# Kernel tuning notes

Measured on AMD Instinct MI355X. Metric: run time of the kernel, lower is better.

The kernel has to match this reference:

```python
import jax, jax.numpy as jnp
import numpy as np

EPS = 1e-6

def setup_inputs() -> dict:
    key = jax.random.key(0)
    k1, k2, k3 = jax.random.split(key, 3)
    B, C, H, W = 2048, 256, 7, 7
    base = jax.random.normal(k1, (B, C, H, W), dtype=jnp.float32)
    moment = jax.random.normal(k2, (B, C, H, W), dtype=jnp.float32)
    A_matrix = jax.random.randint(k3, (B, H * W, H * W), 0, 2, dtype=jnp.int32)
    return {"base": base, "moment": moment, "A_matrix": A_matrix}

def reference(base, moment, A_matrix):
    B, C, H, W = base.shape
    P = H * W  # 49
    b = base.reshape(B, C, P)      # (B, C, 49)
    m = moment.reshape(B, C, P)    # (B, C, 49)
    # pairwise dot over channel dim via batched matmul (avoids BxCx49x49 broadcast)
    dots = jnp.einsum('bcp,bcq->bpq', b, m)            # (B, 49, 49)
    nb = jnp.maximum(jnp.linalg.norm(b, axis=1), EPS)  # (B, 49)
    nm = jnp.maximum(jnp.linalg.norm(m, axis=1), EPS)  # (B, 49)
    cos_sim = dots / (nb[:, :, None] * nm[:, None, :])
    mask = A_matrix.astype(bool)
    # masked mean without dynamic-size gather
    num = jnp.sum(jnp.where(mask, cos_sim, 0.0))
    den = jnp.sum(mask).astype(cos_sim.dtype)
    return -(num / den)
```

## Files before the change

### kernel.cpp

```cpp
#include <hip/hip_runtime.h>
#include <hip/hip_bf16.h>
#include <stdint.h>


typedef __attribute__((ext_vector_type(8))) short short8;
typedef __attribute__((ext_vector_type(4))) float floatx4;

#define P 49
#define CP 12544
#define NMASK 2401
#define MS_STRIDE 72

__device__ __forceinline__ short8 cvt8(float4 a, float4 b) {
  union { __hip_bfloat162 h2; short s2[2]; } t;
  short8 r;
  t.h2 = __float22bfloat162_rn(make_float2(a.x, a.y)); r[0] = t.s2[0]; r[1] = t.s2[1];
  t.h2 = __float22bfloat162_rn(make_float2(a.z, a.w)); r[2] = t.s2[0]; r[3] = t.s2[1];
  t.h2 = __float22bfloat162_rn(make_float2(b.x, b.y)); r[4] = t.s2[0]; r[5] = t.s2[1];
  t.h2 = __float22bfloat162_rn(make_float2(b.z, b.w)); r[6] = t.s2[0]; r[7] = t.s2[1];
  return r;
}

__global__ __launch_bounds__(512, 6) void pixpro_main(
    const float* __restrict__ base, const float* __restrict__ moment,
    const int* __restrict__ A, float* __restrict__ ws_num, float* __restrict__ ws_cnt)
{
  __shared__ __align__(16) uint16_t maskS[P * MS_STRIDE];
  __shared__ __align__(16) float normred[8 * 4 * 64];
  __shared__ __align__(16) float inv_nm_s[64];
  __shared__ __align__(16) float SQred[8 * 4 * 16 * 2];
  __shared__ float cntred[8];

  const int b    = blockIdx.x;
  const int tid  = threadIdx.x;
  const int lane = tid & 63;
  const int wv   = tid >> 6;
  const int mrow = lane & 15;
  const int kgrp = (lane >> 4) & 3;

  const float* gb = base   + (size_t)b * CP;
  const float* gm = moment + (size_t)b * CP;
  const int*   gA = A      + (size_t)b * NMASK;

  short8 afrag[2][2];
  float s0[8], s1[8];
  #pragma unroll
  for (int j = 0; j < 8; ++j) { s0[j] = 0.f; s1[j] = 0.f; }

  #pragma unroll
  for (int cti = 0; cti < 2; ++cti) {
    const int c = (2 * wv + cti) * 16 + mrow;
    const float* row = gm + c * P;
    float4 a0 = *(const float4*)(row + kgrp * 8);
    float4 a1 = *(const float4*)(row + kgrp * 8 + 4);
    float4 b0, b1;
    if (kgrp < 2) {
      b0 = *(const float4*)(row + 32 + kgrp * 8);
      b1 = *(const float4*)(row + 32 + kgrp * 8 + 4);
    } else if (kgrp == 2) {
      b0 = make_float4(row[48], 0.f, 0.f, 0.f);
      b1 = make_float4(0.f, 0.f, 0.f, 0.f);
    } else {
      b0 = make_float4(0.f, 0.f, 0.f, 0.f);
      b1 = make_float4(0.f, 0.f, 0.f, 0.f);
    }
    s0[0] = fmaf(a0.x, a0.x, s0[0]); s0[1] = fmaf(a0.y, a0.y, s0[1]);
    s0[2] = fmaf(a0.z, a0.z, s0[2]); s0[3] = fmaf(a0.w, a0.w, s0[3]);
    s0[4] = fmaf(a1.x, a1.x, s0[4]); s0[5] = fmaf(a1.y, a1.y, s0[5]);
    s0[6] = fmaf(a1.z, a1.z, s0[6]); s0[7] = fmaf(a1.w, a1.w, s0[7]);
    s1[0] = fmaf(b0.x, b0.x, s1[0]); s1[1] = fmaf(b0.y, b0.y, s1[1]);
    s1[2] = fmaf(b0.z, b0.z, s1[2]); s1[3] = fmaf(b0.w, b0.w, s1[3]);
    s1[4] = fmaf(b1.x, b1.x, s1[4]); s1[5] = fmaf(b1.y, b1.y, s1[5]);
    s1[6] = fmaf(b1.z, b1.z, s1[6]); s1[7] = fmaf(b1.w, b1.w, s1[7]);
    afrag[cti][0] = cvt8(a0, a1);
    afrag[cti][1] = cvt8(b0, b1);
  }

  const bool btask = tid < P * 8;
  const int  bp    = tid >> 3;
  const int  bqg   = tid & 7;
  const int  bq0   = bqg * 8;
  int bmask[8];
  #pragma unroll
  for (int j = 0; j < 8; ++j) bmask[j] = 0;
  if (btask) {
    const int* Ar = gA + bp * P + bq0;
    if (bqg <= 5) {
      int4 u0 = *(const int4*)(Ar);
      int4 u1 = *(const int4*)(Ar + 4);
      bmask[0] = u0.x; bmask[1] = u0.y; bmask[2] = u0.z; bmask[3] = u0.w;
      bmask[4] = u1.x; bmask[5] = u1.y; bmask[6] = u1.z; bmask[7] = u1.w;
    } else if (bqg == 6) {
      bmask[0] = Ar[0];
    }
  }

  #pragma unroll
  for (int j = 0; j < 8; ++j) {
    s0[j] += __shfl_xor(s0[j], 1); s0[j] += __shfl_xor(s0[j], 2);
    s1[j] += __shfl_xor(s1[j], 1); s1[j] += __shfl_xor(s1[j], 2);
  }
  if ((lane & 3) == 0) {
    const int h = mrow >> 2;
    float* nb_ = &normred[(wv * 4 + h) * 64 + kgrp * 8];
    *(float4*)(nb_ + 0)  = make_float4(s0[0], s0[1], s0[2], s0[3]);
    *(float4*)(nb_ + 4)  = make_float4(s0[4], s0[5], s0[6], s0[7]);
    *(float4*)(nb_ + 32) = make_float4(s1[0], s1[1], s1[2], s1[3]);
    *(float4*)(nb_ + 36) = make_float4(s1[4], s1[5], s1[6], s1[7]);
  }
  __syncthreads();

  if (tid < 64) {
    float s = 0.f;
    #pragma unroll
    for (int wh = 0; wh < 32; ++wh) s += normred[wh * 64 + tid];
    inv_nm_s[tid] = 1.0f / fmaxf(sqrtf(s), 1e-6f);
  }
  __syncthreads();

  int cntpart = 0;
  if (btask) {
    float4 i0 = *(const float4*)&inv_nm_s[bq0];
    float4 i1 = *(const float4*)&inv_nm_s[bq0 + 4];
    float4 f0, f1;
    f0.x = bmask[0] ? i0.x : 0.f; f0.y = bmask[1] ? i0.y : 0.f;
    f0.z = bmask[2] ? i0.z : 0.f; f0.w = bmask[3] ? i0.w : 0.f;
    f1.x = bmask[4] ? i1.x : 0.f; f1.y = bmask[5] ? i1.y : 0.f;
    f1.z = bmask[6] ? i1.z : 0.f; f1.w = bmask[7] ? i1.w : 0.f;
    #pragma unroll
    for (int j = 0; j < 8; ++j) cntpart += bmask[j];
    *(short8*)&maskS[bp * MS_STRIDE + bq0] = cvt8(f0, f1);
  }
  __syncthreads();

  const int pbase[4] = {0, 16, 32, 33};
  floatx4 acc[2][4];
  #pragma unroll
  for (int i = 0; i < 2; ++i)
    #pragma unroll
    for (int j = 0; j < 4; ++j) acc[i][j] = (floatx4){0.f, 0.f, 0.f, 0.f};

  #pragma unroll
  for (int kt = 0; kt < 2; ++kt) {
    short8 bfr[4];
    #pragma unroll
    for (int pt = 0; pt < 4; ++pt)
      bfr[pt] = *(const short8*)&maskS[(pbase[pt] + mrow) * MS_STRIDE + kt * 32 + kgrp * 8];
    #pragma unroll
    for (int cti = 0; cti < 2; ++cti)
      #pragma unroll
      for (int pt = 0; pt < 4; ++pt)
        acc[cti][pt] = __builtin_amdgcn_mfma_f32_16x16x32_bf16(afrag[cti][kt], bfr[pt], acc[cti][pt], 0, 0, 0);
  }

  float S[4] = {0.f, 0.f, 0.f, 0.f}, Qn[4] = {0.f, 0.f, 0.f, 0.f};
  #pragma unroll
  for (int cti = 0; cti < 2; ++cti) {
    float bv[4][4];
    #pragma unroll
    for (int pt = 0; pt < 4; ++pt) {
      const int pd = pbase[pt] + mrow;
      const bool pv = (pt < 3) || (mrow == 15);
      #pragma unroll
      for (int r = 0; r < 4; ++r) {
        const int c = (2 * wv + cti) * 16 + kgrp * 4 + r;
        float v = gb[c * P + pd];
        bv[pt][r] = pv ? v : 0.f;
      }
    }
    #pragma unroll
    for (int pt = 0; pt < 4; ++pt)
      #pragma unroll
      for (int r = 0; r < 4; ++r) {
        S[pt]  = fmaf(bv[pt][r], acc[cti][pt][r], S[pt]);
        Qn[pt] = fmaf(bv[pt][r], bv[pt][r], Qn[pt]);
      }
  }

  #pragma unroll
  for (int pt = 0; pt < 4; ++pt) {
    S[pt]  += __shfl_xor(S[pt], 16);  S[pt]  += __shfl_xor(S[pt], 32);
    Qn[pt] += __shfl_xor(Qn[pt], 16); Qn[pt] += __shfl_xor(Qn[pt], 32);
  }
  float cntf = (float)cntpart;
  #pragma unroll
  for (int off = 32; off > 0; off >>= 1) cntf += __shfl_xor(cntf, off);

  if (lane < 16) {
    #pragma unroll
    for (int pt = 0; pt < 4; ++pt)
      *(float2*)&SQred[((wv * 4 + pt) * 16 + mrow) * 2] = make_float2(S[pt], Qn[pt]);
  }
  if (lane == 0) cntred[wv] = cntf;
  __syncthreads();

  if (tid < 64) {
    float num = 0.f, cc = 0.f;
    if (tid < P) {
      const int pt = tid >> 4;
      const int mr = (pt == 3) ? 15 : (tid & 15);
      float Sp = 0.f, Qp = 0.f;
      #pragma unroll
      for (int w = 0; w < 8; ++w) {
        const int idx = ((w * 4 + pt) * 16 + mr) * 2;
        Sp += SQred[idx];
        Qp += SQred[idx + 1];
      }
      num = Sp * (1.0f / fmaxf(sqrtf(Qp), 1e-6f));
    }
    if (tid < 8) cc = cntred[tid];
    #pragma unroll
    for (int off = 32; off > 0; off >>= 1) {
      num += __shfl_xor(num, off);
      cc  += __shfl_xor(cc, off);
    }
    if (tid == 0) { ws_num[b] = num; ws_cnt[b] = cc; }
  }
}

__global__ __launch_bounds__(256) void pixpro_reduce(
    const float* __restrict__ ws_num, const float* __restrict__ ws_cnt,
    float* __restrict__ out)
{
  __shared__ float rn[4], rc[4];
  float n = 0.f, c = 0.f;
  for (int i = threadIdx.x; i < 2048; i += 256) { n += ws_num[i]; c += ws_cnt[i]; }
  #pragma unroll
  for (int off = 32; off > 0; off >>= 1) {
    n += __shfl_down(n, off, 64);
    c += __shfl_down(c, off, 64);
  }
  const int wv = threadIdx.x >> 6, lane = threadIdx.x & 63;
  if (lane == 0) { rn[wv] = n; rc[wv] = c; }
  __syncthreads();
  if (threadIdx.x == 0) {
    float N = rn[0] + rn[1] + rn[2] + rn[3];
    float D = rc[0] + rc[1] + rc[2] + rc[3];
    out[0] = -(N / D);
  }
}

extern "C" void kernel_launch(void* const* d_in, const int* in_sizes, int n_in,
                              void* d_out, int out_size, void* d_ws, size_t ws_size,
                              hipStream_t stream) {
  const float* base   = (const float*)d_in[0];
  const float* moment = (const float*)d_in[1];
  const int*   A      = (const int*)d_in[2];
  float* ws_num = (float*)d_ws;
  float* ws_cnt = ws_num + 2048;
  pixpro_main<<<2048, 512, 0, stream>>>(base, moment, A, ws_num, ws_cnt);
  pixpro_reduce<<<1, 256, 0, stream>>>(ws_num, ws_cnt, (float*)d_out);
}
```

Before: 237.7 us.

## Hoist base loads before barriers and fold norm reduction into wave shuffles

All global loads (moment rows, mask, and the 32 scalar base values per thread) are now issued up front, so their latency overlaps the norm reduction and MFMA stages instead of stalling after them. The moment-norm reduction is done more within each wave via extra shuffles, leaving an 8-entry shared buffer. That removes one __syncthreads and the single-wave finalize step; each mask thread now sums the 8 partials and computes the reciprocal norms itself. Register pressure rises, so the occupancy hint drops from 6 to 4 blocks per CU, which may reduce latency hiding.

Result: slower. 264.1 us (+11.1%).

```diff
diff --git a/kernel.cpp b/kernel.cpp
--- a/kernel.cpp
+++ b/kernel.cpp
@@ -21,13 +21,12 @@
   return r;
 }
 
-__global__ __launch_bounds__(512, 6) void pixpro_main(
+__global__ __launch_bounds__(512, 4) void pixpro_main(
     const float* __restrict__ base, const float* __restrict__ moment,
     const int* __restrict__ A, float* __restrict__ ws_num, float* __restrict__ ws_cnt)
 {
   __shared__ __align__(16) uint16_t maskS[P * MS_STRIDE];
-  __shared__ __align__(16) float normred[8 * 4 * 64];
-  __shared__ __align__(16) float inv_nm_s[64];
+  __shared__ __align__(16) float normredW[8 * 64];
   __shared__ __align__(16) float SQred[8 * 4 * 16 * 2];
   __shared__ float cntred[8];
 
@@ -42,28 +41,68 @@
   const float* gm = moment + (size_t)b * CP;
   const int*   gA = A      + (size_t)b * NMASK;
 
-  short8 afrag[2][2];
-  float s0[8], s1[8];
-  #pragma unroll
-  for (int j = 0; j < 8; ++j) { s0[j] = 0.f; s1[j] = 0.f; }
-
+  float4 ma0[2], ma1[2], mb0[2], mb1[2];
   #pragma unroll
   for (int cti = 0; cti < 2; ++cti) {
     const int c = (2 * wv + cti) * 16 + mrow;
     const float* row = gm + c * P;
-    float4 a0 = *(const float4*)(row + kgrp * 8);
-    float4 a1 = *(const float4*)(row + kgrp * 8 + 4);
-    float4 b0, b1;
+    ma0[cti] = *(const float4*)(row + kgrp * 8);
+    ma1[cti] = *(const float4*)(row + kgrp * 8 + 4);
     if (kgrp < 2) {
-      b0 = *(const float4*)(row + 32 + kgrp * 8);
-      b1 = *(const float4*)(row + 32 + kgrp * 8 + 4);
+      mb0[cti] = *(const float4*)(row + 32 + kgrp * 8);
+      mb1[cti] = *(const float4*)(row + 32 + kgrp * 8 + 4);
     } else if (kgrp == 2) {
-      b0 = make_float4(row[48], 0.f, 0.f, 0.f);
-      b1 = make_float4(0.f, 0.f, 0.f, 0.f);
+      mb0[cti] = make_float4(row[48], 0.f, 0.f, 0.f);
+      mb1[cti] = make_float4(0.f, 0.f, 0.f, 0.f);
     } else {
-      b0 = make_float4(0.f, 0.f, 0.f, 0.f);
-      b1 = make_float4(0.f, 0.f, 0.f, 0.f);
-    }
+      mb0[cti] = make_float4(0.f, 0.f, 0.f, 0.f);
+      mb1[cti] = make_float4(0.f, 0.f, 0.f, 0.f);
+    }
+  }
+
+  const bool btask = tid < P * 8;
+  const int  bp    = tid >> 3;
+  const int  bqg   = tid & 7;
+  const int  bq0   = bqg * 8;
+  int bmask[8];
+  #pragma unroll
+  for (int j = 0; j < 8; ++j) bmask[j] = 0;
+  if (btask) {
+    const int* Ar = gA + bp * P + bq0;
+    if (bqg <= 5) {
+      int4 u0 = *(const int4*)(Ar);
+      int4 u1 = *(const int4*)(Ar + 4);
+      bmask[0] = u0.x; bmask[1] = u0.y; bmask[2] = u0.z; bmask[3] = u0.w;
+      bmask[4] = u1.x; bmask[5] = u1.y; bmask[6] = u1.z; bmask[7] = u1.w;
+    } else if (bqg == 6) {
+      bmask[0] = Ar[0];
+    }
+  }
+
+  const int pbase[4] = {0, 16, 32, 33};
+  float bv[2][4][4];
+  #pragma unroll
+  for (int cti = 0; cti < 2; ++cti) {
+    #pragma unroll
+    for (int pt = 0; pt < 4; ++pt) {
+      const int pd = pbase[pt] + mrow;
+      const bool pv = (pt < 3) || (mrow == 15);
+      #pragma unroll
+      for (int r = 0; r < 4; ++r) {
+        const int c = (2 * wv + cti) * 16 + kgrp * 4 + r;
+        float v = gb[c * P + pd];
+        bv[cti][pt][r] = pv ? v : 0.f;
+      }
+    }
+  }
+
+  float s0[8], s1[8];
+  #pragma unroll
+  for (int j = 0; j < 8; ++j) { s0[j] = 0.f; s1[j] = 0.f; }
+  short8 afrag[2][2];
+  #pragma unroll
+  for (int cti = 0; cti < 2; ++cti) {
+    float4 a0 = ma0[cti], a1 = ma1[cti], b0 = mb0[cti], b1 = mb1[cti];
     s0[0] = fmaf(a0.x, a0.x, s0[0]); s0[1] = fmaf(a0.y, a0.y, s0[1]);
     s0[2] = fmaf(a0.z, a0.z, s0[2]); s0[3] = fmaf(a0.w, a0.w, s0[3]);
     s0[4] = fmaf(a1.x, a1.x, s0[4]); s0[5] = fmaf(a1.y, a1.y, s0[5]);
@@ -76,33 +115,15 @@
     afrag[cti][1] = cvt8(b0, b1);
   }
 
-  const bool btask = tid < P * 8;
-  const int  bp    = tid >> 3;
-  const int  bqg   = tid & 7;
-  const int  bq0   = bqg * 8;
-  int bmask[8];
-  #pragma unroll
-  for (int j = 0; j < 8; ++j) bmask[j] = 0;
-  if (btask) {
-    const int* Ar = gA + bp * P + bq0;
-    if (bqg <= 5) {
-      int4 u0 = *(const int4*)(Ar);
-      int4 u1 = *(const int4*)(Ar + 4);
-      bmask[0] = u0.x; bmask[1] = u0.y; bmask[2] = u0.z; bmask[3] = u0.w;
-      bmask[4] = u1.x; bmask[5] = u1.y; bmask[6] = u1.z; bmask[7] = u1.w;
-    } else if (bqg == 6) {
-      bmask[0] = Ar[0];
-    }
-  }
-
   #pragma unroll
   for (int j = 0; j < 8; ++j) {
     s0[j] += __shfl_xor(s0[j], 1); s0[j] += __shfl_xor(s0[j], 2);
+    s0[j] += __shfl_xor(s0[j], 4); s0[j] += __shfl_xor(s0[j], 8);
     s1[j] += __shfl_xor(s1[j], 1); s1[j] += __shfl_xor(s1[j], 2);
-  }
-  if ((lane & 3) == 0) {
-    const int h = mrow >> 2;
-    float* nb_ = &normred[(wv * 4 + h) * 64 + kgrp * 8];
+    s1[j] += __shfl_xor(s1[j], 4); s1[j] += __shfl_xor(s1[j], 8);
+  }
+  if (mrow == 0) {
+    float* nb_ = &normredW[wv * 64 + kgrp * 8];
     *(float4*)(nb_ + 0)  = make_float4(s0[0], s0[1], s0[2], s0[3]);
     *(float4*)(nb_ + 4)  = make_float4(s0[4], s0[5], s0[6], s0[7]);
     *(float4*)(nb_ + 32) = make_float4(s1[0], s1[1], s1[2], s1[3]);
@@ -110,30 +131,33 @@
   }
   __syncthreads();
 
-  if (tid < 64) {
-    float s = 0.f;
-    #pragma unroll
-    for (int wh = 0; wh < 32; ++wh) s += normred[wh * 64 + tid];
-    inv_nm_s[tid] = 1.0f / fmaxf(sqrtf(s), 1e-6f);
-  }
-  __syncthreads();
-
   int cntpart = 0;
   if (btask) {
-    float4 i0 = *(const float4*)&inv_nm_s[bq0];
-    float4 i1 = *(const float4*)&inv_nm_s[bq0 + 4];
+    float4 acc0 = make_float4(0.f, 0.f, 0.f, 0.f);
+    float4 acc1 = make_float4(0.f, 0.f, 0.f, 0.f);
+    #pragma unroll
+    for (int w = 0; w < 8; ++w) {
+      const float* nr = &normredW[w * 64 + bq0];
+      float4 u0 = *(const float4*)(nr);
+      float4 u1 = *(const float4*)(nr + 4);
+      acc0.x += u0.x; acc0.y += u0.y; acc0.z += u0.z; acc0.w += u0.w;
+      acc1.x += u1.x; acc1.y += u1.y; acc1.z += u1.z; acc1.w += u1.w;
+    }
     float4 f0, f1;
-    f0.x = bmask[0] ? i0.x : 0.f; f0.y = bmask[1] ? i0.y : 0.f;
-    f0.z = bmask[2] ? i0.z : 0.f; f0.w = bmask[3] ? i0.w : 0.f;
-    f1.x = bmask[4] ? i1.x : 0.f; f1.y = bmask[5] ? i1.y : 0.f;
-    f1.z = bmask[6] ? i1.z : 0.f; f1.w = bmask[7] ? i1.w : 0.f;
+    f0.x = bmask[0] ? (1.0f / fmaxf(sqrtf(acc0.x), 1e-6f)) : 0.f;
+    f0.y = bmask[1] ? (1.0f / fmaxf(sqrtf(acc0.y), 1e-6f)) : 0.f;
+    f0.z = bmask[2] ? (1.0f / fmaxf(sqrtf(acc0.z), 1e-6f)) : 0.f;
+    f0.w = bmask[3] ? (1.0f / fmaxf(sqrtf(acc0.w), 1e-6f)) : 0.f;
+    f1.x = bmask[4] ? (1.0f / fmaxf(sqrtf(acc1.x), 1e-6f)) : 0.f;
+    f1.y = bmask[5] ? (1.0f / fmaxf(sqrtf(acc1.y), 1e-6f)) : 0.f;
+    f1.z = bmask[6] ? (1.0f / fmaxf(sqrtf(acc1.z), 1e-6f)) : 0.f;
+    f1.w = bmask[7] ? (1.0f / fmaxf(sqrtf(acc1.w), 1e-6f)) : 0.f;
     #pragma unroll
     for (int j = 0; j < 8; ++j) cntpart += bmask[j];
     *(short8*)&maskS[bp * MS_STRIDE + bq0] = cvt8(f0, f1);
   }
   __syncthreads();
 
-  const int pbase[4] = {0, 16, 32, 33};
   floatx4 acc[2][4];
   #pragma unroll
   for (int i = 0; i < 2; ++i)
@@ -155,27 +179,14 @@
 
   float S[4] = {0.f, 0.f, 0.f, 0.f}, Qn[4] = {0.f, 0.f, 0.f, 0.f};
   #pragma unroll
-  for (int cti = 0; cti < 2; ++cti) {
-    float bv[4][4];
-    #pragma unroll
-    for (int pt = 0; pt < 4; ++pt) {
-      const int pd = pbase[pt] + mrow;
-      const bool pv = (pt < 3) || (mrow == 15);
+  for (int cti = 0; cti < 2; ++cti)
+    #pragma unroll
+    for (int pt = 0; pt < 4; ++pt)
       #pragma unroll
       for (int r = 0; r < 4; ++r) {
-        const int c = (2 * wv + cti) * 16 + kgrp * 4 + r;
-        float v = gb[c * P + pd];
-        bv[pt][r] = pv ? v : 0.f;
+        S[pt]  = fmaf(bv[cti][pt][r], acc[cti][pt][r], S[pt]);
+        Qn[pt] = fmaf(bv[cti][pt][r], bv[cti][pt][r], Qn[pt]);
       }
-    }
-    #pragma unroll
-    for (int pt = 0; pt < 4; ++pt)
-      #pragma unroll
-      for (int r = 0; r < 4; ++r) {
-        S[pt]  = fmaf(bv[pt][r], acc[cti][pt][r], S[pt]);
-        Qn[pt] = fmaf(bv[pt][r], bv[pt][r], Qn[pt]);
-      }
-  }
 
   #pragma unroll
   for (int pt = 0; pt < 4; ++pt) {
```

## Compute Gram matrix B^T M via MFMA from transposed LDS tiles, weight after

Applied to the files above, without the earlier changes.

Changes the algorithm from (mask·inv_norm)-weighted moment times base to computing the full 49x49 dot matrix base^T·moment with MFMA over K=256 channels. Both base and moment are staged transposed into LDS as bf16, and the scaled mask is applied afterwards as an elementwise weight. This replaces the strided per-element global base reads and the extra norm passes with coalesced single loads, at the cost of more LDS (lower occupancy target, 4 blocks) and bank-conflicting transposed 16-bit stores. It also rounds base to bf16 before the dot products.

After: 240.2 us. No clear change (+1.0%).

```diff
diff --git a/kernel.cpp b/kernel.cpp
--- a/kernel.cpp
+++ b/kernel.cpp
@@ -9,40 +9,21 @@
 #define P 49
 #define CP 12544
 #define NMASK 2401
-#define MS_STRIDE 72
-
-__device__ __forceinline__ short8 cvt8(float4 a, float4 b) {
-  union { __hip_bfloat162 h2; short s2[2]; } t;
-  short8 r;
-  t.h2 = __float22bfloat162_rn(make_float2(a.x, a.y)); r[0] = t.s2[0]; r[1] = t.s2[1];
-  t.h2 = __float22bfloat162_rn(make_float2(a.z, a.w)); r[2] = t.s2[0]; r[3] = t.s2[1];
-  t.h2 = __float22bfloat162_rn(make_float2(b.x, b.y)); r[4] = t.s2[0]; r[5] = t.s2[1];
-  t.h2 = __float22bfloat162_rn(make_float2(b.z, b.w)); r[6] = t.s2[0]; r[7] = t.s2[1];
-  return r;
-}
-
-__global__ __launch_bounds__(512, 6) void pixpro_main(
-    const float* __restrict__ base, const float* __restrict__ moment,
-    const int* __restrict__ A, float* __restrict__ ws_num, float* __restrict__ ws_cnt)
-{
-  __shared__ __align__(16) uint16_t maskS[P * MS_STRIDE];
-  __shared__ __align__(16) float normred[8 * 4 * 64];
-  __shared__ __align__(16) float inv_nm_s[64];
-  __shared__ __align__(16) float SQred[8 * 4 * 16 * 2];
-  __shared__ float cntred[8];
-
-  const int b    = blockIdx.x;
-  const int tid  = threadIdx.x;
-  const int lane = tid & 63;
-  const int wv   = tid >> 6;
-  const int mrow = lane & 15;
-  const int kgrp = (lane >> 4) & 3;
-
-  const float* gb = base   + (size_t)b * CP;
-  const float* gm = moment + (size_t)b * CP;
-  const int*   gA = A      + (size_t)b * NMASK;
-
-  short8 afrag[2][2];
+#define MT_STRIDE 264
+#define WS_STRIDE 72
+
+__device__ __forceinline__ uint16_t f2bf(float x) {
+  union { float f; uint32_t u; } v; v.f = x;
+  uint32_t r = v.u + 0x7fffu + ((v.u >> 16) & 1u);
+  return (uint16_t)(r >> 16);
+}
+__device__ __forceinline__ float bf2f(uint16_t h) {
+  union { uint32_t u; float f; } v; v.u = ((uint32_t)h) << 16; return v.f;
+}
+
+__device__ __forceinline__ void stage_T(const float* __restrict__ src,
+                                        uint16_t* dstT, float* nred,
+                                        int wv, int mrow, int kgrp) {
   float s0[8], s1[8];
   #pragma unroll
   for (int j = 0; j < 8; ++j) { s0[j] = 0.f; s1[j] = 0.f; }
@@ -50,7 +31,7 @@
   #pragma unroll
   for (int cti = 0; cti < 2; ++cti) {
     const int c = (2 * wv + cti) * 16 + mrow;
-    const float* row = gm + c * P;
+    const float* row = src + c * P;
     float4 a0 = *(const float4*)(row + kgrp * 8);
     float4 a1 = *(const float4*)(row + kgrp * 8 + 4);
     float4 b0, b1;
@@ -72,9 +53,60 @@
     s1[2] = fmaf(b0.z, b0.z, s1[2]); s1[3] = fmaf(b0.w, b0.w, s1[3]);
     s1[4] = fmaf(b1.x, b1.x, s1[4]); s1[5] = fmaf(b1.y, b1.y, s1[5]);
     s1[6] = fmaf(b1.z, b1.z, s1[6]); s1[7] = fmaf(b1.w, b1.w, s1[7]);
-    afrag[cti][0] = cvt8(a0, a1);
-    afrag[cti][1] = cvt8(b0, b1);
-  }
+
+    float av[8] = {a0.x, a0.y, a0.z, a0.w, a1.x, a1.y, a1.z, a1.w};
+    #pragma unroll
+    for (int j = 0; j < 8; ++j)
+      dstT[(kgrp * 8 + j) * MT_STRIDE + c] = f2bf(av[j]);
+    if (kgrp < 2) {
+      float bw[8] = {b0.x, b0.y, b0.z, b0.w, b1.x, b1.y, b1.z, b1.w};
+      #pragma unroll
+      for (int j = 0; j < 8; ++j)
+        dstT[(32 + kgrp * 8 + j) * MT_STRIDE + c] = f2bf(bw[j]);
+    } else if (kgrp == 2) {
+      dstT[48 * MT_STRIDE + c] = f2bf(b0.x);
+    }
+  }
+
+  #pragma unroll
+  for (int j = 0; j < 8; ++j) {
+    s0[j] += __shfl_xor(s0[j], 1); s0[j] += __shfl_xor(s0[j], 2);
+    s0[j] += __shfl_xor(s0[j], 4); s0[j] += __shfl_xor(s0[j], 8);
+    s1[j] += __shfl_xor(s1[j], 1); s1[j] += __shfl_xor(s1[j], 2);
+    s1[j] += __shfl_xor(s1[j], 4); s1[j] += __shfl_xor(s1[j], 8);
+  }
+  if (mrow == 0) {
+    float* nb_ = nred + wv * 64 + kgrp * 8;
+    *(float4*)(nb_ + 0)  = make_float4(s0[0], s0[1], s0[2], s0[3]);
+    *(float4*)(nb_ + 4)  = make_float4(s0[4], s0[5], s0[6], s0[7]);
+    *(float4*)(nb_ + 32) = make_float4(s1[0], s1[1], s1[2], s1[3]);
+    *(float4*)(nb_ + 36) = make_float4(s1[4], s1[5], s1[6], s1[7]);
+  }
+}
+
+__global__ __launch_bounds__(512, 4) void pixpro_main(
+    const float* __restrict__ base, const float* __restrict__ moment,
+    const int* __restrict__ A, float* __restrict__ ws_num, float* __restrict__ ws_cnt)
+{
+  __shared__ __align__(16) uint16_t mT[P * MT_STRIDE];
+  __shared__ __align__(16) uint16_t bT[P * MT_STRIDE];
+  __shared__ __align__(16) float nredM[8 * 64];
+  __shared__ __align__(16) float nredB[8 * 64];
+  __shared__ __align__(16) uint16_t wS[P * WS_STRIDE];
+  __shared__ float numredS[8], cntredS[8];
+
+  const int b    = blockIdx.x;
+  const int tid  = threadIdx.x;
+  const int lane = tid & 63;
+  const int wv   = tid >> 6;
+  const int mrow = lane & 15;
+  const int kgrp = (lane >> 4) & 3;
+
+  const float* gb = base   + (size_t)b * CP;
+  const float* gm = moment + (size_t)b * CP;
+  const int*   gA = A      + (size_t)b * NMASK;
+
+  stage_T(gm, mT, nredM, wv, mrow, kgrp);
 
   const bool btask = tid < P * 8;
   const int  bp    = tid >> 3;
@@ -95,126 +127,101 @@
     }
   }
 
-  #pragma unroll
-  for (int j = 0; j < 8; ++j) {
-    s0[j] += __shfl_xor(s0[j], 1); s0[j] += __shfl_xor(s0[j], 2);
-    s1[j] += __shfl_xor(s1[j], 1); s1[j] += __shfl_xor(s1[j], 2);
-  }
-  if ((lane & 3) == 0) {
-    const int h = mrow >> 2;
-    float* nb_ = &normred[(wv * 4 + h) * 64 + kgrp * 8];
-    *(float4*)(nb_ + 0)  = make_float4(s0[0], s0[1], s0[2], s0[3]);
-    *(float4*)(nb_ + 4)  = make_float4(s0[4], s0[5], s0[6], s0[7]);
-    *(float4*)(nb_ + 32) = make_float4(s1[0], s1[1], s1[2], s1[3]);
-    *(float4*)(nb_ + 36) = make_float4(s1[4], s1[5], s1[6], s1[7]);
-  }
-  __syncthreads();
-
-  if (tid < 64) {
-    float s = 0.f;
-    #pragma unroll
-    for (int wh = 0; wh < 32; ++wh) s += normred[wh * 64 + tid];
-    inv_nm_s[tid] = 1.0f / fmaxf(sqrtf(s), 1e-6f);
-  }
+  stage_T(gb, bT, nredB, wv, mrow, kgrp);
+
   __syncthreads();
 
   int cntpart = 0;
   if (btask) {
-    float4 i0 = *(const float4*)&inv_nm_s[bq0];
-    float4 i1 = *(const float4*)&inv_nm_s[bq0 + 4];
-    float4 f0, f1;
-    f0.x = bmask[0] ? i0.x : 0.f; f0.y = bmask[1] ? i0.y : 0.f;
-    f0.z = bmask[2] ? i0.z : 0.f; f0.w = bmask[3] ? i0.w : 0.f;
-    f1.x = bmask[4] ? i1.x : 0.f; f1.y = bmask[5] ? i1.y : 0.f;
-    f1.z = bmask[6] ? i1.z : 0.f; f1.w = bmask[7] ? i1.w : 0.f;
+    float4 a0 = make_float4(0.f, 0.f, 0.f, 0.f);
+    float4 a1 = make_float4(0.f, 0.f, 0.f, 0.f);
+    float nb2 = 0.f;
+    #pragma unroll
+    for (int w = 0; w < 8; ++w) {
+      const float* nr = &nredM[w * 64 + bq0];
+      float4 u0 = *(const float4*)(nr);
+      float4 u1 = *(const float4*)(nr + 4);
+      a0.x += u0.x; a0.y += u0.y; a0.z += u0.z; a0.w += u0.w;
+      a1.x += u1.x; a1.y += u1.y; a1.z += u1.z; a1.w += u1.w;
+      nb2 += nredB[w * 64 + bp];
+    }
+    const float inb = 1.0f / fmaxf(sqrtf(nb2), 1e-6f);
+    float wf[8];
+    wf[0] = bmask[0] ? inb * (1.0f / fmaxf(sqrtf(a0.x), 1e-6f)) : 0.f;
+    wf[1] = bmask[1] ? inb * (1.0f / fmaxf(sqrtf(a0.y), 1e-6f)) : 0.f;
+    wf[2] = bmask[2] ? inb * (1.0f / fmaxf(sqrtf(a0.z), 1e-6f)) : 0.f;
+    wf[3] = bmask[3] ? inb * (1.0f / fmaxf(sqrtf(a0.w), 1e-6f)) : 0.f;
+    wf[4] = bmask[4] ? inb * (1.0f / fmaxf(sqrtf(a1.x), 1e-6f)) : 0.f;
+    wf[5] = bmask[5] ? inb * (1.0f / fmaxf(sqrtf(a1.y), 1e-6f)) : 0.f;
+    wf[6] = bmask[6] ? inb * (1.0f / fmaxf(sqrtf(a1.z), 1e-6f)) : 0.f;
+    wf[7] = bmask[7] ? inb * (1.0f / fmaxf(sqrtf(a1.w), 1e-6f)) : 0.f;
     #pragma unroll
     for (int j = 0; j < 8; ++j) cntpart += bmask[j];
-    *(short8*)&maskS[bp * MS_STRIDE + bq0] = cvt8(f0, f1);
-  }
-  __syncthreads();
-
-  const int pbase[4] = {0, 16, 32, 33};
-  floatx4 acc[2][4];
-  #pragma unroll
-  for (int i = 0; i < 2; ++i)
-    #pragma unroll
-    for (int j = 0; j < 4; ++j) acc[i][j] = (floatx4){0.f, 0.f, 0.f, 0.f};
-
-  #pragma unroll
-  for (int kt = 0; kt < 2; ++kt) {
-    short8 bfr[4];
-    #pragma unroll
-    for (int pt = 0; pt < 4; ++pt)
-      bfr[pt] = *(const short8*)&maskS[(pbase[pt] + mrow) * MS_STRIDE + kt * 32 + kgrp * 8];
-    #pragma unroll
-    for (int cti = 0; cti < 2; ++cti)
-      #pragma unroll
-      for (int pt = 0; pt < 4; ++pt)
-        acc[cti][pt] = __builtin_amdgcn_mfma_f32_16x16x32_bf16(afrag[cti][kt], bfr[pt], acc[cti][pt], 0, 0, 0);
-  }
-
-  float S[4] = {0.f, 0.f, 0.f, 0.f}, Qn[4] = {0.f, 0.f, 0.f, 0.f};
-  #pragma unroll
-  for (int cti = 0; cti < 2; ++cti) {
-    float bv[4][4];
-    #pragma unroll
-    for (int pt = 0; pt < 4; ++pt) {
-      const int pd = pbase[pt] + mrow;
-      const bool pv = (pt < 3) || (mrow == 15);
-      #pragma unroll
-      for (int r = 0; r < 4; ++r) {
-        const int c = (2 * wv + cti) * 16 + kgrp * 4 + r;
-        float v = gb[c * P + pd];
-        bv[pt][r] = pv ? v : 0.f;
-      }
-    }
-    #pragma unroll
-    for (int pt = 0; pt < 4; ++pt)
-      #pragma unroll
-      for (int r = 0; r < 4; ++r) {
-        S[pt]  = fmaf(bv[pt][r], acc[cti][pt][r], S[pt]);
-        Qn[pt] = fmaf(bv[pt][r], bv[pt][r], Qn[pt]);
-      }
-  }
-
-  #pragma unroll
-  for (int pt = 0; pt < 4; ++pt) {
-    S[pt]  += __shfl_xor(S[pt], 16);  S[pt]  += __shfl_xor(S[pt], 32);
-    Qn[pt] += __shfl_xor(Qn[pt], 16); Qn[pt] += __shfl_xor(Qn[pt], 32);
-  }
+    short8 w8;
+    #pragma unroll
+    for (int j = 0; j < 8; ++j) w8[j] = (short)f2bf(wf[j]);
+    *(short8*)&wS[bp * WS_STRIDE + bq0] = w8;
+  }
+
+  const int pt  = wv & 3;
+  const int qt1i = 2 * (wv >> 2) + 1;
+  const int pbaseV  = (pt < 3) ? pt * 16 : 33;
+  const int qbase0  = (qt1i - 1) * 16;
+  const int qbase1  = (qt1i < 3) ? qt1i * 16 : 33;
+
+  const int arow  = (pbaseV + mrow) * MT_STRIDE;
+  const int brow0 = (qbase0 + mrow) * MT_STRIDE;
+  const int brow1 = (qbase1 + mrow) * MT_STRIDE;
+
+  floatx4 acc0 = (floatx4){0.f, 0.f, 0.f, 0.f};
+  floatx4 acc1 = (floatx4){0.f, 0.f, 0.f, 0.f};
+  #pragma unroll
+  for (int ks = 0; ks < 8; ++ks) {
+    const int off = ks * 32 + kgrp * 8;
+    short8 af  = *(const short8*)&bT[arow  + off];
+    short8 bf0 = *(const short8*)&mT[brow0 + off];
+    short8 bf1 = *(const short8*)&mT[brow1 + off];
+    acc0 = __builtin_amdgcn_mfma_f32_16x16x32_bf16(af, bf0, acc0, 0, 0, 0);
+    acc1 = __builtin_amdgcn_mfma_f32_16x16x32_bf16(af, bf1, acc1, 0, 0, 0);
+  }
+
+  __syncthreads();
+
+  const bool vq1 = (qt1i < 3) || (mrow == 15);
+  const int  q0r = qbase0 + mrow;
+  const int  q1r = qbase1 + mrow;
+  float numpart = 0.f;
+  #pragma unroll
+  for (int r = 0; r < 4; ++r) {
+    const int rr = kgrp * 4 + r;
+    const int p  = pbaseV + rr;
+    const bool vp = (pt < 3) || (rr == 15);
+    if (vp) {
+      float w0 = bf2f(wS[p * WS_STRIDE + q0r]);
+      float w1 = vq1 ? bf2f(wS[p * WS_STRIDE + q1r]) : 0.f;
+      numpart = fmaf(w0, acc0[r], numpart);
+      numpart = fmaf(w1, acc1[r], numpart);
+    }
+  }
+
   float cntf = (float)cntpart;
   #pragma unroll
-  for (int off = 32; off > 0; off >>= 1) cntf += __shfl_xor(cntf, off);
-
-  if (lane < 16) {
-    #pragma unroll
-    for (int pt = 0; pt < 4; ++pt)
-      *(float2*)&SQred[((wv * 4 + pt) * 16 + mrow) * 2] = make_float2(S[pt], Qn[pt]);
-  }
-  if (lane == 0) cntred[wv] = cntf;
+  for (int off = 32; off > 0; off >>= 1) {
+    numpart += __shfl_xor(numpart, off);
+    cntf    += __shfl_xor(cntf, off);
+  }
+  if (lane == 0) { numredS[wv] = numpart; cntredS[wv] = cntf; }
   __syncthreads();
 
   if (tid < 64) {
-    float num = 0.f, cc = 0.f;
-    if (tid < P) {
-      const int pt = tid >> 4;
-      const int mr = (pt == 3) ? 15 : (tid & 15);
-      float Sp = 0.f, Qp = 0.f;
-      #pragma unroll
-      for (int w = 0; w < 8; ++w) {
-        const int idx = ((w * 4 + pt) * 16 + mr) * 2;
-        Sp += SQred[idx];
-        Qp += SQred[idx + 1];
-      }
-      num = Sp * (1.0f / fmaxf(sqrtf(Qp), 1e-6f));
-    }
-    if (tid < 8) cc = cntred[tid];
-    #pragma unroll
-    for (int off = 32; off > 0; off >>= 1) {
-      num += __shfl_xor(num, off);
-      cc  += __shfl_xor(cc, off);
-    }
-    if (tid == 0) { ws_num[b] = num; ws_cnt[b] = cc; }
+    float n = (tid < 8) ? numredS[tid] : 0.f;
+    float c = (tid < 8) ? cntredS[tid] : 0.f;
+    #pragma unroll
+    for (int off = 4; off > 0; off >>= 1) {
+      n += __shfl_xor(n, off);
+      c += __shfl_xor(c, off);
+    }
+    if (tid == 0) { ws_num[b] = n; ws_cnt[b] = c; }
   }
 }
 
```

## Split channel-norm computation into a separate pre-pass kernel

Applied to the files above, without the earlier changes.

Moves the per-pixel L2 norms of base and moment into a new pixpro_norms kernel that writes inverse norms to workspace. The gram kernel reads those instead of reducing norms through shared memory, which drops two barriers and the Qn accumulation. It also folds the base inverse norm into a single per-thread scalar reduction. The cost is a full second read of base and moment plus an extra launch, in exchange for a shorter, less synchronised main kernel.

New measurement: 285.1 us. 19.9% more time.

```diff
diff --git a/kernel.cpp b/kernel.cpp
--- a/kernel.cpp
+++ b/kernel.cpp
@@ -21,15 +21,43 @@
   return r;
 }
 
-__global__ __launch_bounds__(512, 6) void pixpro_main(
+__global__ __launch_bounds__(512, 8) void pixpro_norms(
     const float* __restrict__ base, const float* __restrict__ moment,
-    const int* __restrict__ A, float* __restrict__ ws_num, float* __restrict__ ws_cnt)
+    float* __restrict__ invb_g, float* __restrict__ invm_g)
+{
+  const int b   = blockIdx.x;
+  const int tid = threadIdx.x;
+  const int q   = tid >> 3;
+  const int cg  = tid & 7;
+  float am = 0.f, ab = 0.f;
+  if (q < P) {
+    const float* pm = moment + (size_t)b * CP + (cg * 32) * P + q;
+    const float* pb = base   + (size_t)b * CP + (cg * 32) * P + q;
+    #pragma unroll
+    for (int i = 0; i < 32; ++i) {
+      const float vm = pm[i * P];
+      const float vb = pb[i * P];
+      am = fmaf(vm, vm, am);
+      ab = fmaf(vb, vb, ab);
+    }
+  }
+  am += __shfl_xor(am, 1); am += __shfl_xor(am, 2); am += __shfl_xor(am, 4);
+  ab += __shfl_xor(ab, 1); ab += __shfl_xor(ab, 2); ab += __shfl_xor(ab, 4);
+  if (cg == 0 && q < P) {
+    invm_g[b * 64 + q] = 1.0f / fmaxf(sqrtf(am), 1e-6f);
+    invb_g[b * 64 + q] = 1.0f / fmaxf(sqrtf(ab), 1e-6f);
+  }
+}
+
+__global__ __launch_bounds__(512, 6) void pixpro_gram(
+    const float* __restrict__ base, const float* __restrict__ moment,
+    const int* __restrict__ A, const float* __restrict__ invb_g,
+    const float* __restrict__ invm_g,
+    float* __restrict__ ws_num, float* __restrict__ ws_cnt)
 {
   __shared__ __align__(16) uint16_t maskS[P * MS_STRIDE];
-  __shared__ __align__(16) float normred[8 * 4 * 64];
-  __shared__ __align__(16) float inv_nm_s[64];
-  __shared__ __align__(16) float SQred[8 * 4 * 16 * 2];
-  __shared__ float cntred[8];
+  __shared__ __align__(16) float invBs[52];
+  __shared__ float numred[8], cntred[8];
 
   const int b    = blockIdx.x;
   const int tid  = threadIdx.x;
@@ -43,10 +71,6 @@
   const int*   gA = A      + (size_t)b * NMASK;
 
   short8 afrag[2][2];
-  float s0[8], s1[8];
-  #pragma unroll
-  for (int j = 0; j < 8; ++j) { s0[j] = 0.f; s1[j] = 0.f; }
-
   #pragma unroll
   for (int cti = 0; cti < 2; ++cti) {
     const int c = (2 * wv + cti) * 16 + mrow;
@@ -64,14 +88,6 @@
       b0 = make_float4(0.f, 0.f, 0.f, 0.f);
       b1 = make_float4(0.f, 0.f, 0.f, 0.f);
     }
-    s0[0] = fmaf(a0.x, a0.x, s0[0]); s0[1] = fmaf(a0.y, a0.y, s0[1]);
-    s0[2] = fmaf(a0.z, a0.z, s0[2]); s0[3] = fmaf(a0.w, a0.w, s0[3]);
-    s0[4] = fmaf(a1.x, a1.x, s0[4]); s0[5] = fmaf(a1.y, a1.y, s0[5]);
-    s0[6] = fmaf(a1.z, a1.z, s0[6]); s0[7] = fmaf(a1.w, a1.w, s0[7]);
-    s1[0] = fmaf(b0.x, b0.x, s1[0]); s1[1] = fmaf(b0.y, b0.y, s1[1]);
-    s1[2] = fmaf(b0.z, b0.z, s1[2]); s1[3] = fmaf(b0.w, b0.w, s1[3]);
-    s1[4] = fmaf(b1.x, b1.x, s1[4]); s1[5] = fmaf(b1.y, b1.y, s1[5]);
-    s1[6] = fmaf(b1.z, b1.z, s1[6]); s1[7] = fmaf(b1.w, b1.w, s1[7]);
     afrag[cti][0] = cvt8(a0, a1);
     afrag[cti][1] = cvt8(b0, b1);
   }
@@ -95,33 +111,12 @@
     }
   }
 
-  #pragma unroll
-  for (int j = 0; j < 8; ++j) {
-    s0[j] += __shfl_xor(s0[j], 1); s0[j] += __shfl_xor(s0[j], 2);
-    s1[j] += __shfl_xor(s1[j], 1); s1[j] += __shfl_xor(s1[j], 2);
-  }
-  if ((lane & 3) == 0) {
-    const int h = mrow >> 2;
-    float* nb_ = &normred[(wv * 4 + h) * 64 + kgrp * 8];
-    *(float4*)(nb_ + 0)  = make_float4(s0[0], s0[1], s0[2], s0[3]);
-    *(float4*)(nb_ + 4)  = make_float4(s0[4], s0[5], s0[6], s0[7]);
-    *(float4*)(nb_ + 32) = make_float4(s1[0], s1[1], s1[2], s1[3]);
-    *(float4*)(nb_ + 36) = make_float4(s1[4], s1[5], s1[6], s1[7]);
-  }
-  __syncthreads();
-
-  if (tid < 64) {
-    float s = 0.f;
-    #pragma unroll
-    for (int wh = 0; wh < 32; ++wh) s += normred[wh * 64 + tid];
-    inv_nm_s[tid] = 1.0f / fmaxf(sqrtf(s), 1e-6f);
-  }
-  __syncthreads();
+  if (tid < P) invBs[tid] = invb_g[b * 64 + tid];
 
   int cntpart = 0;
   if (btask) {
-    float4 i0 = *(const float4*)&inv_nm_s[bq0];
-    float4 i1 = *(const float4*)&inv_nm_s[bq0 + 4];
+    float4 i0 = *(const float4*)(invm_g + b * 64 + bq0);
+    float4 i1 = *(const float4*)(invm_g + b * 64 + bq0 + 4);
     float4 f0, f1;
     f0.x = bmask[0] ? i0.x : 0.f; f0.y = bmask[1] ? i0.y : 0.f;
     f0.z = bmask[2] ? i0.z : 0.f; f0.w = bmask[3] ? i0.w : 0.f;
@@ -153,68 +148,46 @@
         acc[cti][pt] = __builtin_amdgcn_mfma_f32_16x16x32_bf16(afrag[cti][kt], bfr[pt], acc[cti][pt], 0, 0, 0);
   }
 
-  float S[4] = {0.f, 0.f, 0.f, 0.f}, Qn[4] = {0.f, 0.f, 0.f, 0.f};
-  #pragma unroll
-  for (int cti = 0; cti < 2; ++cti) {
-    float bv[4][4];
+  float numpart = 0.f;
+  {
+    float invp[4];
     #pragma unroll
     for (int pt = 0; pt < 4; ++pt) {
       const int pd = pbase[pt] + mrow;
       const bool pv = (pt < 3) || (mrow == 15);
+      invp[pt] = pv ? invBs[pd] : 0.f;
+    }
+    #pragma unroll
+    for (int cti = 0; cti < 2; ++cti)
       #pragma unroll
-      for (int r = 0; r < 4; ++r) {
-        const int c = (2 * wv + cti) * 16 + kgrp * 4 + r;
-        float v = gb[c * P + pd];
-        bv[pt][r] = pv ? v : 0.f;
+      for (int pt = 0; pt < 4; ++pt) {
+        const int pd = pbase[pt] + mrow;
+        #pragma unroll
+        for (int r = 0; r < 4; ++r) {
+          const int c = (2 * wv + cti) * 16 + kgrp * 4 + r;
+          numpart = fmaf(invp[pt] * gb[c * P + pd], acc[cti][pt][r], numpart);
+        }
       }
-    }
-    #pragma unroll
-    for (int pt = 0; pt < 4; ++pt)
-      #pragma unroll
-      for (int r = 0; r < 4; ++r) {
-        S[pt]  = fmaf(bv[pt][r], acc[cti][pt][r], S[pt]);
-        Qn[pt] = fmaf(bv[pt][r], bv[pt][r], Qn[pt]);
-      }
-  }
-
-  #pragma unroll
-  for (int pt = 0; pt < 4; ++pt) {
-    S[pt]  += __shfl_xor(S[pt], 16);  S[pt]  += __shfl_xor(S[pt], 32);
-    Qn[pt] += __shfl_xor(Qn[pt], 16); Qn[pt] += __shfl_xor(Qn[pt], 32);
-  }
+  }
+
   float cntf = (float)cntpart;
   #pragma unroll
-  for (int off = 32; off > 0; off >>= 1) cntf += __shfl_xor(cntf, off);
-
-  if (lane < 16) {
-    #pragma unroll
-    for (int pt = 0; pt < 4; ++pt)
-      *(float2*)&SQred[((wv * 4 + pt) * 16 + mrow) * 2] = make_float2(S[pt], Qn[pt]);
-  }
-  if (lane == 0) cntred[wv] = cntf;
+  for (int off = 32; off > 0; off >>= 1) {
+    numpart += __shfl_xor(numpart, off);
+    cntf    += __shfl_xor(cntf, off);
+  }
+  if (lane == 0) { numred[wv] = numpart; cntred[wv] = cntf; }
   __syncthreads();
 
   if (tid < 64) {
-    float num = 0.f, cc = 0.f;
-    if (tid < P) {
-      const int pt = tid >> 4;
-      const int mr = (pt == 3) ? 15 : (tid & 15);
-      float Sp = 0.f, Qp = 0.f;
-      #pragma unroll
-      for (int w = 0; w < 8; ++w) {
-        const int idx = ((w * 4 + pt) * 16 + mr) * 2;
-        Sp += SQred[idx];
-        Qp += SQred[idx + 1];
-      }
-      num = Sp * (1.0f / fmaxf(sqrtf(Qp), 1e-6f));
-    }
-    if (tid < 8) cc = cntred[tid];
-    #pragma unroll
-    for (int off = 32; off > 0; off >>= 1) {
-      num += __shfl_xor(num, off);
-      cc  += __shfl_xor(cc, off);
-    }
-    if (tid == 0) { ws_num[b] = num; ws_cnt[b] = cc; }
+    float n = (tid < 8) ? numred[tid] : 0.f;
+    float c = (tid < 8) ? cntred[tid] : 0.f;
+    #pragma unroll
+    for (int off = 4; off > 0; off >>= 1) {
+      n += __shfl_xor(n, off);
+      c += __shfl_xor(c, off);
+    }
+    if (tid == 0) { ws_num[b] = n; ws_cnt[b] = c; }
   }
 }
 
@@ -248,6 +221,9 @@
   const int*   A      = (const int*)d_in[2];
   float* ws_num = (float*)d_ws;
   float* ws_cnt = ws_num + 2048;
-  pixpro_main<<<2048, 512, 0, stream>>>(base, moment, A, ws_num, ws_cnt);
+  float* invb_g = ws_cnt + 2048;
+  float* invm_g = invb_g + 2048 * 64;
+  pixpro_norms<<<2048, 512, 0, stream>>>(base, moment, invb_g, invm_g);
+  pixpro_gram<<<2048, 512, 0, stream>>>(base, moment, A, invb_g, invm_g, ws_num, ws_cnt);
   pixpro_reduce<<<1, 256, 0, stream>>>(ws_num, ws_cnt, (float*)d_out);
 }
```
